# Performance work log

Hardware: AMD Instinct MI355X
Metric: run time of the kernel (lower is better)

Reference implementation:

```python
import jax, jax.numpy as jnp
import numpy as np

C = 128

def setup_inputs() -> dict:
    key = jax.random.key(0)
    ks = jax.random.split(key, 7)
    s = 1.0 / np.sqrt(C)
    return {
        "x": jax.random.normal(ks[0], (8, C, 64, 64), dtype=jnp.float32),
        "Wq": jax.random.uniform(ks[1], (C, C), jnp.float32, -s, s),
        "bq": jax.random.uniform(ks[2], (C,), jnp.float32, -s, s),
        "Wk": jax.random.uniform(ks[3], (C, C), jnp.float32, -s, s),
        "bk": jax.random.uniform(ks[4], (C,), jnp.float32, -s, s),
        "Wv": jax.random.uniform(ks[5], (C, C), jnp.float32, -s, s),
        "bv": jax.random.uniform(ks[6], (C,), jnp.float32, -s, s),
    }

def reference(x, Wq, bq, Wk, bk, Wv, bv):
    bs, c, h, w = x.shape
    xf = x.reshape(bs, c, h * w)                      # [B, C, N]
    # 1x1 convs == per-pixel linear maps over channels
    q = jnp.einsum("dc,bcn->bdn", Wq, xf) + bq[None, :, None]
    k = jnp.einsum("dc,bcn->bdn", Wk, xf) + bk[None, :, None]
    v = jnp.einsum("dc,bcn->bdn", Wv, xf) + bv[None, :, None]
    # energy[b,i,j] = <q[:,i], k[:,j]>  (no 1/sqrt(d) scaling, per original)
    energy = jnp.einsum("bci,bcj->bij", q, k)         # [B, N, N]
    attn = jax.nn.softmax(energy, axis=-1)
    # out[b,c,i] = sum_j v[b,c,j] * attn[b,i,j]
    out = jnp.einsum("bcj,bij->bci", v, attn)
    return out.reshape(bs, c, h, w)
```

## Files before the change

kernel.cpp:

```cpp
#include <hip/hip_runtime.h>
#include <stdint.h>
#include <math.h>

typedef float  f32x4  __attribute__((ext_vector_type(4)));
typedef float  f32x16 __attribute__((ext_vector_type(16)));
typedef short  bf16x8 __attribute__((ext_vector_type(8)));
typedef unsigned int u32;
typedef unsigned int u32x4 __attribute__((ext_vector_type(4)));
typedef unsigned short ushort_t;

#define MFMA32(a, b, c) __builtin_amdgcn_mfma_f32_32x32x16_bf16((a), (b), (c), 0, 0, 0)

constexpr int B_ = 8, C_ = 128, N_ = 4096;
constexpr float LOG2E = 1.44269504088896340736f;

__device__ __forceinline__ u32 pack2bf(float a, float b) {
  u32 ua = __builtin_bit_cast(u32, a);
  u32 ub = __builtin_bit_cast(u32, b);
  ua += 0x7fffu + ((ua >> 16) & 1u);
  ub += 0x7fffu + ((ub >> 16) & 1u);
  return (ua >> 16) | (ub & 0xffff0000u);
}
__device__ __forceinline__ bf16x8 pack8(const float* v, float s) {
  u32x4 d = { pack2bf(v[0]*s, v[1]*s), pack2bf(v[2]*s, v[3]*s),
              pack2bf(v[4]*s, v[5]*s), pack2bf(v[6]*s, v[7]*s) };
  return __builtin_bit_cast(bf16x8, d);
}

__global__ __launch_bounds__(256)
void wprep_kernel(const float* __restrict__ Wq, const float* __restrict__ Wk,
                  const float* __restrict__ Wv, ushort_t* __restrict__ Wf)
{
  const int tid  = blockIdx.x * 256 + threadIdx.x;
  const int widx = tid >> 11;
  const int r    = tid & 2047;
  const int dt   = r >> 9;
  const int kc   = (r >> 6) & 7;
  const int ln   = r & 63;
  const float* W = (widx == 0) ? Wq : (widx == 1) ? Wk : Wv;
  const float s  = (widx == 0) ? LOG2E : 1.0f;
  const int d    = dt * 32 + (ln & 31);
  const int c0   = kc * 16 + (ln >> 5) * 8;
  const float* p = W + d * C_ + c0;
  f32x4 lo = *(const f32x4*)p, hi = *(const f32x4*)(p + 4);
  float v[8] = { lo.x, lo.y, lo.z, lo.w, hi.x, hi.y, hi.z, hi.w };
  *(bf16x8*)(Wf + (size_t)tid * 8) = pack8(v, s);
}

__global__ __launch_bounds__(256, 2)
void proj_kernel(const float* __restrict__ x,
                 const float* __restrict__ bq, const float* __restrict__ bk,
                 const float* __restrict__ bv, const ushort_t* __restrict__ Wf,
                 ushort_t* __restrict__ Qf, ushort_t* __restrict__ Kf,
                 ushort_t* __restrict__ Vf)
{
  const int b   = blockIdx.x & 7;
  const int n0  = (blockIdx.x >> 3) << 6;
  const int t   = threadIdx.x;
  const int w   = t >> 6;
  const int lane = t & 63;
  const int l31 = t & 31;
  const int lq1 = (t >> 5) & 1;
  const int pb  = w & 1;
  const int pix = n0 + pb * 32 + l31;

  bf16x8 xf[8];
#pragma unroll
  for (int kc = 0; kc < 8; ++kc) {
    float v[8];
#pragma unroll
    for (int e = 0; e < 8; ++e)
      v[e] = x[(size_t)(b * C_ + kc * 16 + lq1 * 8 + e) * N_ + pix];
    xf[kc] = pack8(v, 1.0f);
  }

  const ushort_t* WQf = Wf;
  const ushort_t* WKf = Wf + 16384;
  const ushort_t* WVf = Wf + 32768;
  const f32x16 Z = {0,0,0,0,0,0,0,0,0,0,0,0,0,0,0,0};

  if (w < 2) {
    const int i32 = (n0 >> 5) + pb;
#pragma unroll
    for (int dt = 0; dt < 4; ++dt) {
      f32x16 sq = Z, sk = Z;
#pragma unroll
      for (int kc = 0; kc < 8; ++kc) {
        bf16x8 wq = *(const bf16x8*)(WQf + (size_t)(dt * 8 + kc) * 512 + lane * 8);
        bf16x8 wk = *(const bf16x8*)(WKf + (size_t)(dt * 8 + kc) * 512 + lane * 8);
        sq = MFMA32(wq, xf[kc], sq);
        sk = MFMA32(wk, xf[kc], sk);
      }
#pragma unroll
      for (int q = 0; q < 4; ++q) {
        const int dbase = dt * 32 + q * 8 + lq1 * 4;
        f32x4 b4q = *(const f32x4*)(bq + dbase);
        f32x4 b4k = *(const f32x4*)(bk + dbase);
        uint2 qs, ks;
        qs.x = pack2bf(sq[4*q+0] + b4q.x * LOG2E, sq[4*q+1] + b4q.y * LOG2E);
        qs.y = pack2bf(sq[4*q+2] + b4q.z * LOG2E, sq[4*q+3] + b4q.w * LOG2E);
        ks.x = pack2bf(sk[4*q+0] + b4k.x, sk[4*q+1] + b4k.y);
        ks.y = pack2bf(sk[4*q+2] + b4k.z, sk[4*q+3] + b4k.w);
        const int kcf = dt * 2 + (q >> 1), h = q & 1;
        const size_t off = ((size_t)((b * 128 + i32) * 8 + kcf) * 64 + h * 32 + l31) * 8 + lq1 * 4;
        *(uint2*)(Qf + off) = qs;
        *(uint2*)(Kf + off) = ks;
      }
    }
  } else {
#pragma unroll
    for (int dt = 0; dt < 4; ++dt) {
      f32x16 sv = Z;
#pragma unroll
      for (int kc = 0; kc < 8; ++kc) {
        bf16x8 wv = *(const bf16x8*)(WVf + (size_t)(dt * 8 + kc) * 512 + lane * 8);
        sv = MFMA32(xf[kc], wv, sv);
      }
      const float bvl = bv[dt * 32 + l31];
#pragma unroll
      for (int q = 0; q < 4; ++q) {
        uint2 vs;
        vs.x = pack2bf(sv[4*q+0] + bvl, sv[4*q+1] + bvl);
        vs.y = pack2bf(sv[4*q+2] + bvl, sv[4*q+3] + bvl);
        const int j64 = n0 >> 6;
        const int j16 = pb * 2 + (q >> 1);
        const size_t off = ((size_t)((b * 64 + j64) * 4 + dt) * 4 + j16) * 512 +
                           (size_t)((q & 1) * 32 + l31) * 8 + lq1 * 4;
        *(uint2*)(Vf + off) = vs;
      }
    }
  }
}

__global__ __launch_bounds__(256, 2)
void flash_kernel(const ushort_t* __restrict__ Qf, const ushort_t* __restrict__ Kf,
                  const ushort_t* __restrict__ Vf, float* __restrict__ out,
                  float* __restrict__ opart, float* __restrict__ lpart, int js)
{
  const int b     = blockIdx.x & 7;
  const int itile = (blockIdx.x >> 3) & 31;
  const int jsl   = blockIdx.x >> 8;
  const int t     = threadIdx.x;
  const int wv    = t >> 6;
  const int lane  = t & 63;
  const int l31   = t & 31;
  const int lq1   = (t >> 5) & 1;
  const int i0    = itile * 128 + wv * 32;

  __shared__ short smem[16384];

  bf16x8 qf[8];
  const size_t qbase = (size_t)((b * 128 + (i0 >> 5)) * 8) * 512;
#pragma unroll
  for (int kc = 0; kc < 8; ++kc)
    qf[kc] = *(const bf16x8*)(Qf + qbase + (size_t)kc * 512 + lane * 8);

  const f32x16 Z = {0,0,0,0,0,0,0,0,0,0,0,0,0,0,0,0};
  f32x16 o[4] = {Z, Z, Z, Z};
  float lsum = 0.f;

  const int tpj = 64 / js, rem = 64 % js;
  const int jt0 = jsl * tpj + (jsl < rem ? jsl : rem);
  const int jtn = tpj + (jsl < rem ? 1 : 0);

  const ushort_t* Kt0 = Kf + (size_t)(b * 128) * 4096;
  const ushort_t* Vt0 = Vf + (size_t)(b * 64) * 8192;

  for (int jt = jt0; jt < jt0 + jtn; ++jt) {
    const ushort_t* ksrc = Kt0 + (size_t)jt * 8192;
    const ushort_t* vsrc = Vt0 + (size_t)jt * 8192;
    bf16x8 tmp[8];
#pragma unroll
    for (int c = 0; c < 4; ++c)
      tmp[c] = *(const bf16x8*)(ksrc + (size_t)(c * 256 + t) * 8);
#pragma unroll
    for (int c = 0; c < 4; ++c)
      tmp[4 + c] = *(const bf16x8*)(vsrc + (size_t)(c * 256 + t) * 8);
    __syncthreads();
#pragma unroll
    for (int c = 0; c < 8; ++c)
      *(bf16x8*)(smem + (size_t)(c * 256 + t) * 8) = tmp[c];
    __syncthreads();

#pragma unroll
    for (int jblk = 0; jblk < 2; ++jblk) {
      f32x16 s = Z;
#pragma unroll
      for (int kc = 0; kc < 8; ++kc) {
        bf16x8 kf = *(const bf16x8*)(smem + (jblk * 8 + kc) * 512 + lane * 8);
        s = MFMA32(kf, qf[kc], s);
      }
#pragma unroll
      for (int half = 0; half < 2; ++half) {
        const int cc = jblk * 2 + half;
        const int rb = half * 8;
        float e0 = exp2f(s[rb+0]), e1 = exp2f(s[rb+1]);
        float e2 = exp2f(s[rb+2]), e3 = exp2f(s[rb+3]);
        float e4 = exp2f(s[rb+4]), e5 = exp2f(s[rb+5]);
        float e6 = exp2f(s[rb+6]), e7 = exp2f(s[rb+7]);
        lsum += ((e0 + e1) + (e2 + e3)) + ((e4 + e5) + (e6 + e7));

        u32 a  = pack2bf(e0, e1), b2 = pack2bf(e2, e3);
        u32 c2 = pack2bf(e4, e5), d2 = pack2bf(e6, e7);
        u32 ap = __shfl_xor(a, 32),  bp = __shfl_xor(b2, 32);
        u32 cp = __shfl_xor(c2, 32), dp = __shfl_xor(d2, 32);
        u32x4 fr = lq1 ? (u32x4){cp, dp, c2, d2} : (u32x4){a, b2, ap, bp};
        bf16x8 pa = __builtin_bit_cast(bf16x8, fr);

#pragma unroll
        for (int ct = 0; ct < 4; ++ct) {
          bf16x8 vf = *(const bf16x8*)(smem + 8192 + (ct * 4 + cc) * 512 + lane * 8);
          o[ct] = MFMA32(pa, vf, o[ct]);
        }
      }
    }
  }

  lsum += __shfl_xor(lsum, 32);

  if (js == 1) {
    const float inv = 1.0f / lsum;
#pragma unroll
    for (int ct = 0; ct < 4; ++ct)
#pragma unroll
      for (int q = 0; q < 4; ++q) {
        f32x4 ov;
#pragma unroll
        for (int r = 0; r < 4; ++r)
          ov[r] = o[ct][4*q+r] * __shfl(inv, lq1 * 4 + q * 8 + r);
        *(f32x4*)(out + (size_t)(b * C_ + ct * 32 + l31) * N_ +
                  i0 + lq1 * 4 + q * 8) = ov;
      }
  } else {
    float* op = opart + (size_t)jsl * B_ * C_ * N_;
#pragma unroll
    for (int ct = 0; ct < 4; ++ct)
#pragma unroll
      for (int q = 0; q < 4; ++q) {
        f32x4 ov = { o[ct][4*q+0], o[ct][4*q+1], o[ct][4*q+2], o[ct][4*q+3] };
        *(f32x4*)(op + (size_t)(b * C_ + ct * 32 + l31) * N_ +
                  i0 + lq1 * 4 + q * 8) = ov;
      }
    if (lane < 32)
      lpart[(size_t)jsl * B_ * N_ + (size_t)b * N_ + i0 + l31] = lsum;
  }
}

__global__ __launch_bounds__(256)
void combine_kernel(const float* __restrict__ opart, const float* __restrict__ lpart,
                    float* __restrict__ out, int js)
{
  const int t  = blockIdx.x * 256 + threadIdx.x;
  const int n4 = (t & 1023) * 4;
  const int bc = t >> 10;
  const int b  = bc >> 7;
  const size_t off  = (size_t)bc * N_ + n4;
  const size_t loff = (size_t)b * N_ + n4;
  f32x4 os = {0,0,0,0}, ls = {0,0,0,0};
  for (int s = 0; s < js; ++s) {
    os += *(const f32x4*)(opart + (size_t)s * B_ * C_ * N_ + off);
    ls += *(const f32x4*)(lpart + (size_t)s * B_ * N_ + loff);
  }
  f32x4 r = { os.x / ls.x, os.y / ls.y, os.z / ls.z, os.w / ls.w };
  *(f32x4*)(out + off) = r;
}

extern "C" void kernel_launch(void* const* d_in, const int* in_sizes, int n_in,
                              void* d_out, int out_size, void* d_ws, size_t ws_size,
                              hipStream_t stream) {
  const float* x  = (const float*)d_in[0];
  const float* Wq = (const float*)d_in[1];
  const float* bq = (const float*)d_in[2];
  const float* Wk = (const float*)d_in[3];
  const float* bk = (const float*)d_in[4];
  const float* Wv = (const float*)d_in[5];
  const float* bv = (const float*)d_in[6];
  float* out = (float*)d_out;

  const size_t nc = (size_t)B_ * N_ * C_;
  ushort_t* qf = (ushort_t*)d_ws;
  ushort_t* kf = qf + nc;
  ushort_t* vf = kf + nc;
  ushort_t* wf = vf + nc;
  const size_t base = (3 * nc + 49152) * sizeof(ushort_t);

  auto need = [&](int jss) {
    return base + (size_t)jss * ((size_t)B_ * N_ + (size_t)B_ * C_ * N_) * 4;
  };
  const int js = (ws_size >= need(2)) ? 2 : 1;

  float* lpart = (float*)((char*)d_ws + base);
  float* opart = lpart + (size_t)js * B_ * N_;

  hipLaunchKernelGGL(wprep_kernel, dim3(24), dim3(256), 0, stream, Wq, Wk, Wv, wf);
  hipLaunchKernelGGL(proj_kernel, dim3(512), dim3(256), 0, stream,
                     x, bq, bk, bv, wf, qf, kf, vf);
  hipLaunchKernelGGL(flash_kernel, dim3(256 * js), dim3(256), 0, stream,
                     qf, kf, vf, out, opart, lpart, js);
  if (js > 1)
    hipLaunchKernelGGL(combine_kernel, dim3(4096), dim3(256), 0, stream,
                       opart, lpart, out, js);
}
```

Measured before the change: 202.6 us.

## Double query rows per wave, read V from global, split keys four ways

The flash kernel now gives each wave 64 query rows (two Q blocks), so every K and V fragment feeds two MFMAs. V fragments are read straight from global memory instead of being staged in shared memory, which halves LDS use. The key split rises to 4 when workspace allows, and the first split writes directly into the output buffer to save one partial buffer. The projection kernel stages x through padded shared memory for coalesced loads, and bf16 packing of P uses a cheaper round-half-up perm. The cost is more registers (which may lower occupancy), uncached global V reads, and scalar strided output stores.

```diff
diff --git a/kernel.cpp b/kernel.cpp
--- a/kernel.cpp
+++ b/kernel.cpp
@@ -20,6 +20,11 @@
   ua += 0x7fffu + ((ua >> 16) & 1u);
   ub += 0x7fffu + ((ub >> 16) & 1u);
   return (ua >> 16) | (ub & 0xffff0000u);
+}
+__device__ __forceinline__ u32 pkfast(float a, float b) {
+  u32 ua = __builtin_bit_cast(u32, a) + 0x8000u;
+  u32 ub = __builtin_bit_cast(u32, b) + 0x8000u;
+  return __builtin_amdgcn_perm(ub, ua, 0x07060302u);
 }
 __device__ __forceinline__ bf16x8 pack8(const float* v, float s) {
   u32x4 d = { pack2bf(v[0]*s, v[1]*s), pack2bf(v[2]*s, v[3]*s),
@@ -62,7 +67,20 @@
   const int l31 = t & 31;
   const int lq1 = (t >> 5) & 1;
   const int pb  = w & 1;
-  const int pix = n0 + pb * 32 + l31;
+
+  __shared__ float xs[128 * 65];
+  {
+    const float* xb = x + (size_t)b * C_ * N_ + n0;
+    const int m  = t & 15;
+    const int cb = t >> 4;
+#pragma unroll
+    for (int it = 0; it < 8; ++it) {
+      const int c = it * 16 + cb;
+      f32x4 v = *(const f32x4*)(xb + (size_t)c * N_ + m * 4);
+      *(f32x4*)&xs[c * 65 + m * 4] = v;
+    }
+  }
+  __syncthreads();
 
   bf16x8 xf[8];
 #pragma unroll
@@ -70,7 +88,7 @@
     float v[8];
 #pragma unroll
     for (int e = 0; e < 8; ++e)
-      v[e] = x[(size_t)(b * C_ + kc * 16 + lq1 * 8 + e) * N_ + pix];
+      v[e] = xs[(kc * 16 + lq1 * 8 + e) * 65 + pb * 32 + l31];
     xf[kc] = pack8(v, 1.0f);
   }
 
@@ -80,7 +98,10 @@
   const f32x16 Z = {0,0,0,0,0,0,0,0,0,0,0,0,0,0,0,0};
 
   if (w < 2) {
+    const int pix = n0 + pb * 32 + l31;
     const int i32 = (n0 >> 5) + pb;
+    const size_t rowoff = ((size_t)b * N_ + pix) * C_;
+    (void)rowoff;
 #pragma unroll
     for (int dt = 0; dt < 4; ++dt) {
       f32x16 sq = Z, sk = Z;
@@ -123,8 +144,8 @@
         vs.x = pack2bf(sv[4*q+0] + bvl, sv[4*q+1] + bvl);
         vs.y = pack2bf(sv[4*q+2] + bvl, sv[4*q+3] + bvl);
         const int j64 = n0 >> 6;
-        const int j16 = pb * 2 + (q >> 1);
-        const size_t off = ((size_t)((b * 64 + j64) * 4 + dt) * 4 + j16) * 512 +
+        const int cc  = pb * 2 + (q >> 1);
+        const size_t off = ((size_t)((b * 64 + j64) * 4 + dt) * 4 + cc) * 512 +
                            (size_t)((q & 1) * 32 + l31) * 8 + lq1 * 4;
         *(uint2*)(Vf + off) = vs;
       }
@@ -135,114 +156,128 @@
 __global__ __launch_bounds__(256, 2)
 void flash_kernel(const ushort_t* __restrict__ Qf, const ushort_t* __restrict__ Kf,
                   const ushort_t* __restrict__ Vf, float* __restrict__ out,
-                  float* __restrict__ opart, float* __restrict__ lpart, int js)
+                  float* __restrict__ opart, float* __restrict__ lpart,
+                  int js, int tiles_per)
 {
   const int b     = blockIdx.x & 7;
-  const int itile = (blockIdx.x >> 3) & 31;
-  const int jsl   = blockIdx.x >> 8;
+  const int itile = (blockIdx.x >> 3) & 15;
+  const int jsl   = blockIdx.x >> 7;
   const int t     = threadIdx.x;
   const int wv    = t >> 6;
   const int lane  = t & 63;
   const int l31   = t & 31;
   const int lq1   = (t >> 5) & 1;
-  const int i0    = itile * 128 + wv * 32;
-
-  __shared__ short smem[16384];
-
-  bf16x8 qf[8];
-  const size_t qbase = (size_t)((b * 128 + (i0 >> 5)) * 8) * 512;
-#pragma unroll
-  for (int kc = 0; kc < 8; ++kc)
-    qf[kc] = *(const bf16x8*)(Qf + qbase + (size_t)kc * 512 + lane * 8);
+  const int i0    = itile * 256 + wv * 64;
+
+  __shared__ short ks_s[8192];
+
+  bf16x8 qf[2][8];
+#pragma unroll
+  for (int iblk = 0; iblk < 2; ++iblk)
+#pragma unroll
+    for (int kc = 0; kc < 8; ++kc)
+      qf[iblk][kc] = *(const bf16x8*)(Qf +
+          ((size_t)((b * 128 + (i0 >> 5) + iblk) * 8 + kc)) * 512 + lane * 8);
 
   const f32x16 Z = {0,0,0,0,0,0,0,0,0,0,0,0,0,0,0,0};
-  f32x16 o[4] = {Z, Z, Z, Z};
-  float lsum = 0.f;
-
-  const int tpj = 64 / js, rem = 64 % js;
-  const int jt0 = jsl * tpj + (jsl < rem ? jsl : rem);
-  const int jtn = tpj + (jsl < rem ? 1 : 0);
-
-  const ushort_t* Kt0 = Kf + (size_t)(b * 128) * 4096;
-  const ushort_t* Vt0 = Vf + (size_t)(b * 64) * 8192;
-
-  for (int jt = jt0; jt < jt0 + jtn; ++jt) {
+  f32x16 o[2][4] = {{Z,Z,Z,Z},{Z,Z,Z,Z}};
+  float ls0 = 0.f, ls1 = 0.f;
+
+  const int jt0 = jsl * tiles_per;
+  const ushort_t* Kt0 = Kf + (size_t)b * 524288;
+  const ushort_t* Vt0 = Vf + (size_t)b * 524288;
+
+  for (int jt = jt0; jt < jt0 + tiles_per; ++jt) {
     const ushort_t* ksrc = Kt0 + (size_t)jt * 8192;
+    bf16x8 tmp[4];
+#pragma unroll
+    for (int c = 0; c < 4; ++c)
+      tmp[c] = *(const bf16x8*)(ksrc + (size_t)(wv * 4 + c) * 512 + lane * 8);
+    __syncthreads();
+#pragma unroll
+    for (int c = 0; c < 4; ++c)
+      *(bf16x8*)&ks_s[(wv * 4 + c) * 512 + lane * 8] = tmp[c];
+    __syncthreads();
+
     const ushort_t* vsrc = Vt0 + (size_t)jt * 8192;
-    bf16x8 tmp[8];
-#pragma unroll
-    for (int c = 0; c < 4; ++c)
-      tmp[c] = *(const bf16x8*)(ksrc + (size_t)(c * 256 + t) * 8);
-#pragma unroll
-    for (int c = 0; c < 4; ++c)
-      tmp[4 + c] = *(const bf16x8*)(vsrc + (size_t)(c * 256 + t) * 8);
-    __syncthreads();
-#pragma unroll
-    for (int c = 0; c < 8; ++c)
-      *(bf16x8*)(smem + (size_t)(c * 256 + t) * 8) = tmp[c];
-    __syncthreads();
-
 #pragma unroll
     for (int jblk = 0; jblk < 2; ++jblk) {
-      f32x16 s = Z;
+      f32x16 s0 = Z, s1 = Z;
 #pragma unroll
       for (int kc = 0; kc < 8; ++kc) {
-        bf16x8 kf = *(const bf16x8*)(smem + (jblk * 8 + kc) * 512 + lane * 8);
-        s = MFMA32(kf, qf[kc], s);
+        bf16x8 kf = *(const bf16x8*)&ks_s[(jblk * 8 + kc) * 512 + lane * 8];
+        s0 = MFMA32(kf, qf[0][kc], s0);
+        s1 = MFMA32(kf, qf[1][kc], s1);
+      }
+      bf16x8 pa[2][2];
+#pragma unroll
+      for (int half = 0; half < 2; ++half) {
+        const int rb = half * 8;
+#pragma unroll
+        for (int iblk = 0; iblk < 2; ++iblk) {
+          const f32x16 sv = iblk ? s1 : s0;
+          float e0 = exp2f(sv[rb+0]), e1 = exp2f(sv[rb+1]);
+          float e2 = exp2f(sv[rb+2]), e3 = exp2f(sv[rb+3]);
+          float e4 = exp2f(sv[rb+4]), e5 = exp2f(sv[rb+5]);
+          float e6 = exp2f(sv[rb+6]), e7 = exp2f(sv[rb+7]);
+          const float rs = ((e0+e1)+(e2+e3)) + ((e4+e5)+(e6+e7));
+          if (iblk) ls1 += rs; else ls0 += rs;
+          u32 a  = pkfast(e0, e1), b2 = pkfast(e2, e3);
+          u32 c2 = pkfast(e4, e5), d2 = pkfast(e6, e7);
+          u32 ap = __shfl_xor(a, 32),  bp = __shfl_xor(b2, 32);
+          u32 cp = __shfl_xor(c2, 32), dp = __shfl_xor(d2, 32);
+          u32x4 fr = lq1 ? (u32x4){cp, dp, c2, d2} : (u32x4){a, b2, ap, bp};
+          pa[iblk][half] = __builtin_bit_cast(bf16x8, fr);
+        }
       }
 #pragma unroll
       for (int half = 0; half < 2; ++half) {
         const int cc = jblk * 2 + half;
-        const int rb = half * 8;
-        float e0 = exp2f(s[rb+0]), e1 = exp2f(s[rb+1]);
-        float e2 = exp2f(s[rb+2]), e3 = exp2f(s[rb+3]);
-        float e4 = exp2f(s[rb+4]), e5 = exp2f(s[rb+5]);
-        float e6 = exp2f(s[rb+6]), e7 = exp2f(s[rb+7]);
-        lsum += ((e0 + e1) + (e2 + e3)) + ((e4 + e5) + (e6 + e7));
-
-        u32 a  = pack2bf(e0, e1), b2 = pack2bf(e2, e3);
-        u32 c2 = pack2bf(e4, e5), d2 = pack2bf(e6, e7);
-        u32 ap = __shfl_xor(a, 32),  bp = __shfl_xor(b2, 32);
-        u32 cp = __shfl_xor(c2, 32), dp = __shfl_xor(d2, 32);
-        u32x4 fr = lq1 ? (u32x4){cp, dp, c2, d2} : (u32x4){a, b2, ap, bp};
-        bf16x8 pa = __builtin_bit_cast(bf16x8, fr);
-
 #pragma unroll
         for (int ct = 0; ct < 4; ++ct) {
-          bf16x8 vf = *(const bf16x8*)(smem + 8192 + (ct * 4 + cc) * 512 + lane * 8);
-          o[ct] = MFMA32(pa, vf, o[ct]);
+          bf16x8 vf = *(const bf16x8*)(vsrc + (size_t)(ct * 4 + cc) * 512 + lane * 8);
+          o[0][ct] = MFMA32(vf, pa[0][half], o[0][ct]);
+          o[1][ct] = MFMA32(vf, pa[1][half], o[1][ct]);
         }
       }
     }
   }
 
-  lsum += __shfl_xor(lsum, 32);
+  ls0 += __shfl_xor(ls0, 32);
+  ls1 += __shfl_xor(ls1, 32);
 
   if (js == 1) {
-    const float inv = 1.0f / lsum;
-#pragma unroll
-    for (int ct = 0; ct < 4; ++ct)
-#pragma unroll
-      for (int q = 0; q < 4; ++q) {
-        f32x4 ov;
-#pragma unroll
-        for (int r = 0; r < 4; ++r)
-          ov[r] = o[ct][4*q+r] * __shfl(inv, lq1 * 4 + q * 8 + r);
-        *(f32x4*)(out + (size_t)(b * C_ + ct * 32 + l31) * N_ +
-                  i0 + lq1 * 4 + q * 8) = ov;
-      }
+    const float inv0 = 1.0f / ls0, inv1 = 1.0f / ls1;
+#pragma unroll
+    for (int iblk = 0; iblk < 2; ++iblk) {
+      const float inv = iblk ? inv1 : inv0;
+      const int ib = i0 + iblk * 32 + l31;
+#pragma unroll
+      for (int ct = 0; ct < 4; ++ct)
+#pragma unroll
+        for (int rg = 0; rg < 16; ++rg) {
+          const int c = ct * 32 + (rg >> 2) * 8 + lq1 * 4 + (rg & 3);
+          out[(size_t)(b * C_ + c) * N_ + ib] = o[iblk][ct][rg] * inv;
+        }
+    }
   } else {
-    float* op = opart + (size_t)jsl * B_ * C_ * N_;
-#pragma unroll
-    for (int ct = 0; ct < 4; ++ct)
-#pragma unroll
-      for (int q = 0; q < 4; ++q) {
-        f32x4 ov = { o[ct][4*q+0], o[ct][4*q+1], o[ct][4*q+2], o[ct][4*q+3] };
-        *(f32x4*)(op + (size_t)(b * C_ + ct * 32 + l31) * N_ +
-                  i0 + lq1 * 4 + q * 8) = ov;
-      }
-    if (lane < 32)
-      lpart[(size_t)jsl * B_ * N_ + (size_t)b * N_ + i0 + l31] = lsum;
+    float* op = jsl ? (opart + (size_t)(jsl - 1) * B_ * C_ * N_) : out;
+#pragma unroll
+    for (int iblk = 0; iblk < 2; ++iblk) {
+      const int ib = i0 + iblk * 32 + l31;
+#pragma unroll
+      for (int ct = 0; ct < 4; ++ct)
+#pragma unroll
+        for (int rg = 0; rg < 16; ++rg) {
+          const int c = ct * 32 + (rg >> 2) * 8 + lq1 * 4 + (rg & 3);
+          op[(size_t)(b * C_ + c) * N_ + ib] = o[iblk][ct][rg];
+        }
+    }
+    if (lane < 32) {
+      float* lp = lpart + (size_t)jsl * B_ * N_ + (size_t)b * N_;
+      lp[i0 + l31]      = ls0;
+      lp[i0 + 32 + l31] = ls1;
+    }
   }
 }
 
@@ -256,9 +291,10 @@
   const int b  = bc >> 7;
   const size_t off  = (size_t)bc * N_ + n4;
   const size_t loff = (size_t)b * N_ + n4;
-  f32x4 os = {0,0,0,0}, ls = {0,0,0,0};
-  for (int s = 0; s < js; ++s) {
-    os += *(const f32x4*)(opart + (size_t)s * B_ * C_ * N_ + off);
+  f32x4 os = *(const f32x4*)(out + off);
+  f32x4 ls = *(const f32x4*)(lpart + loff);
+  for (int s = 1; s < js; ++s) {
+    os += *(const f32x4*)(opart + (size_t)(s - 1) * B_ * C_ * N_ + off);
     ls += *(const f32x4*)(lpart + (size_t)s * B_ * N_ + loff);
   }
   f32x4 r = { os.x / ls.x, os.y / ls.y, os.z / ls.z, os.w / ls.w };
@@ -285,9 +321,10 @@
   const size_t base = (3 * nc + 49152) * sizeof(ushort_t);
 
   auto need = [&](int jss) {
-    return base + (size_t)jss * ((size_t)B_ * N_ + (size_t)B_ * C_ * N_) * 4;
+    return base + (size_t)jss * (size_t)B_ * N_ * 4 +
+           (size_t)(jss - 1) * (size_t)B_ * C_ * N_ * 4;
   };
-  const int js = (ws_size >= need(2)) ? 2 : 1;
+  const int js = (ws_size >= need(4)) ? 4 : (ws_size >= need(2)) ? 2 : 1;
 
   float* lpart = (float*)((char*)d_ws + base);
   float* opart = lpart + (size_t)js * B_ * N_;
@@ -295,8 +332,8 @@
   hipLaunchKernelGGL(wprep_kernel, dim3(24), dim3(256), 0, stream, Wq, Wk, Wv, wf);
   hipLaunchKernelGGL(proj_kernel, dim3(512), dim3(256), 0, stream,
                      x, bq, bk, bv, wf, qf, kf, vf);
-  hipLaunchKernelGGL(flash_kernel, dim3(256 * js), dim3(256), 0, stream,
-                     qf, kf, vf, out, opart, lpart, js);
+  hipLaunchKernelGGL(flash_kernel, dim3(128 * js), dim3(256), 0, stream,
+                     qf, kf, vf, out, opart, lpart, js, 64 / js);
   if (js > 1)
     hipLaunchKernelGGL(combine_kernel, dim3(4096), dim3(256), 0, stream,
                        opart, lpart, out, js);
```

New measurement: 260.8 us. 1.29x slower.
